# Performance work log

Hardware: AMD Instinct MI355X
Metric: run time of the kernel (lower is better)

The kernel has to match this reference:

```python
import jax, jax.numpy as jnp
import numpy as np

B, S_Q, S_KV = 4, 2048, 2048
D_MODEL, HEADS, D_QK, D_V = 1024, 16, 64, 64


def setup_inputs() -> dict:
    key = jax.random.key(0)
    ks = jax.random.split(key, 12)
    s = lambda fan_in: 1.0 / np.sqrt(fan_in)
    return {
        "x": jax.random.normal(ks[0], (B, S_Q, D_MODEL), jnp.float32),
        "encoder_output": jax.random.normal(ks[1], (B, S_KV, D_MODEL), jnp.float32),
        # per-head Linear weights stacked over heads: [H, D_MODEL, d_head]
        "Wq": jax.random.uniform(ks[2], (HEADS, D_MODEL, D_QK), jnp.float32, -s(D_MODEL), s(D_MODEL)),
        "bq": jax.random.uniform(ks[3], (HEADS, D_QK), jnp.float32, -s(D_MODEL), s(D_MODEL)),
        "Wk": jax.random.uniform(ks[4], (HEADS, D_MODEL, D_QK), jnp.float32, -s(D_MODEL), s(D_MODEL)),
        "bk": jax.random.uniform(ks[5], (HEADS, D_QK), jnp.float32, -s(D_MODEL), s(D_MODEL)),
        "Wv": jax.random.uniform(ks[6], (HEADS, D_MODEL, D_V), jnp.float32, -s(D_MODEL), s(D_MODEL)),
        "bv": jax.random.uniform(ks[7], (HEADS, D_V), jnp.float32, -s(D_MODEL), s(D_MODEL)),
        # output Linear: [H*D_V, D_MODEL]
        "Wo": jax.random.uniform(ks[8], (HEADS * D_V, D_MODEL), jnp.float32, -s(HEADS * D_V), s(HEADS * D_V)),
        "bo": jax.random.uniform(ks[9], (D_MODEL,), jnp.float32, -s(HEADS * D_V), s(HEADS * D_V)),
    }


def reference(x, encoder_output, Wq, bq, Wk, bk, Wv, bv, Wo, bo):
    # Batched equivalent of the per-head Python loop: project all heads at once.
    q = jnp.einsum("bqd,hde->bhqe", x, Wq) + bq[None, :, None, :]              # [B,H,Sq,dk]
    k = jnp.einsum("bsd,hde->bhse", encoder_output, Wk) + bk[None, :, None, :]  # [B,H,Skv,dk]
    v = jnp.einsum("bsd,hde->bhse", encoder_output, Wv) + bv[None, :, None, :]  # [B,H,Skv,dv]
    scale = 1.0 / jnp.sqrt(jnp.asarray(D_QK, x.dtype))
    scores = jnp.einsum("bhqe,bhse->bhqs", q, k) * scale                        # [B,H,Sq,Skv]
    attn = jax.nn.softmax(scores, axis=-1)
    heads = jnp.einsum("bhqs,bhse->bhqe", attn, v)                              # [B,H,Sq,dv]
    # concat heads on last dim (head order matches the torch list concat)
    multihead = heads.transpose(0, 2, 1, 3).reshape(x.shape[0], x.shape[1], HEADS * D_V)
    return multihead @ Wo + bo
```

## Files before the change

kernel.cpp:

```cpp
#include <hip/hip_runtime.h>
#include <hip/hip_bf16.h>
#include <stdint.h>

typedef unsigned short u16;
typedef __bf16 bf16x8 __attribute__((ext_vector_type(8)));
typedef float f32x4 __attribute__((ext_vector_type(4)));
typedef float f32x16 __attribute__((ext_vector_type(16)));
typedef unsigned short us8 __attribute__((ext_vector_type(8)));

__device__ __forceinline__ u16 f2bf(float f) {
  union { float f; uint32_t u; } v; v.f = f;
  uint32_t u = v.u;
  return (u16)((u + 0x7FFFu + ((u >> 16) & 1u)) >> 16);
}

__device__ __forceinline__ uint32_t cvtpk(float a, float b) {
  uint32_t r;
  asm("v_cvt_pk_bf16_f32 %0, %1, %2" : "=v"(r) : "v"(a), "v"(b));
  return r;
}

__device__ __forceinline__ void gload_lds16(const void* g, void* l) {
  __builtin_amdgcn_global_load_lds(
      (const __attribute__((address_space(1))) void*)(uintptr_t)g,
      (__attribute__((address_space(3))) void*)(uint32_t)(uintptr_t)l,
      16, 0, 0);
}

__device__ __forceinline__ float vsum16(f32x16 v) {
  float a = (v[0] + v[1]) + (v[2] + v[3]);
  float b = (v[4] + v[5]) + (v[6] + v[7]);
  float c = (v[8] + v[9]) + (v[10] + v[11]);
  float d = (v[12] + v[13]) + (v[14] + v[15]);
  return (a + b) + (c + d);
}

#define CROW(r, g) (((r) & 3) + 8 * ((r) >> 2) + 4 * (g))


__global__ __launch_bounds__(256) void f32_to_bf16_k(const float* __restrict__ in,
                                                     u16* __restrict__ out) {
  size_t i = (size_t)blockIdx.x * 256 + threadIdx.x;
  const float4* p = (const float4*)in + i * 2;
  float4 a = p[0], b = p[1];
  us8 o;
  o[0] = f2bf(a.x); o[1] = f2bf(a.y); o[2] = f2bf(a.z); o[3] = f2bf(a.w);
  o[4] = f2bf(b.x); o[5] = f2bf(b.y); o[6] = f2bf(b.z); o[7] = f2bf(b.w);
  *(us8*)(out + i * 8) = o;
}

__global__ __launch_bounds__(256) void cvt_wqkv_k(const float* __restrict__ Wq,
                                                  const float* __restrict__ Wk,
                                                  const float* __restrict__ Wv,
                                                  u16* __restrict__ oq, u16* __restrict__ ok,
                                                  u16* __restrict__ ov) {
  __shared__ float t[64][65];
  int z = blockIdx.z;
  const float* W = (z == 0) ? Wq : (z == 1) ? Wk : Wv;
  u16* o = (z == 0) ? oq : (z == 1) ? ok : ov;
  const int h = blockIdx.y, d0 = blockIdx.x * 64;
  const int tid = threadIdx.x;
  const float* Wb = W + ((size_t)h << 16) + (size_t)d0 * 64;
#pragma unroll
  for (int i = 0; i < 4; ++i) {
    int idx = tid + i * 256;
    int dl = idx >> 4, e4 = (idx & 15) << 2;
    float4 v = *(const float4*)(Wb + dl * 64 + e4);
    t[dl][e4 + 0] = v.x; t[dl][e4 + 1] = v.y; t[dl][e4 + 2] = v.z; t[dl][e4 + 3] = v.w;
  }
  __syncthreads();
#pragma unroll
  for (int i = 0; i < 2; ++i) {
    int idx = tid + i * 256;
    int e = idx >> 3, dc = (idx & 7) * 8;
    us8 w;
#pragma unroll
    for (int j = 0; j < 8; ++j) w[j] = f2bf(t[dc + j][e]);
    *(us8*)(o + ((size_t)(h * 64 + e)) * 1024 + d0 + dc) = w;
  }
}

__global__ __launch_bounds__(256) void cvt_wo_k(const float* __restrict__ Wo,
                                                u16* __restrict__ o) {
  __shared__ float t[64][65];
  const int k0 = blockIdx.x * 64, n0 = blockIdx.y * 64;
  const int tid = threadIdx.x;
  const float* Wb = Wo + (size_t)k0 * 1024 + n0;
#pragma unroll
  for (int i = 0; i < 4; ++i) {
    int idx = tid + i * 256;
    int kl = idx >> 4, n4 = (idx & 15) << 2;
    float4 v = *(const float4*)(Wb + (size_t)kl * 1024 + n4);
    t[kl][n4 + 0] = v.x; t[kl][n4 + 1] = v.y; t[kl][n4 + 2] = v.z; t[kl][n4 + 3] = v.w;
  }
  __syncthreads();
#pragma unroll
  for (int i = 0; i < 2; ++i) {
    int idx = tid + i * 256;
    int n = idx >> 3, kc = (idx & 7) * 8;
    us8 w;
#pragma unroll
    for (int j = 0; j < 8; ++j) w[j] = f2bf(t[kc + j][n]);
    *(us8*)(o + ((size_t)(n0 + n)) * 1024 + k0 + kc) = w;
  }
}

template <int MODE>
__global__ __launch_bounds__(256) void gemm_bt_k(const u16* __restrict__ A,
                                                 const u16* __restrict__ B,
                                                 const float* __restrict__ bias,
                                                 void* __restrict__ C, int M, int N, int K,
                                                 float scale) {
  __shared__ __attribute__((aligned(16))) u16 As[128 * 32];
  __shared__ __attribute__((aligned(16))) u16 Bs[128 * 32];
  const int tid = threadIdx.x;
  const int wave = tid >> 6, lane = tid & 63;
  const int lo = lane & 15, hi = lane >> 4;
  const int n0 = blockIdx.x * 128, m0 = blockIdx.y * 128;
  const int wr = wave >> 1, wc = wave & 1;

  f32x4 acc[4][4] = {};

  const int o0 = wave * 1024 + lane * 16;
  const int r0 = o0 >> 6, cb0 = o0 & 63;
  const int o1 = o0 + 4096;
  const int r1 = o1 >> 6, cb1 = o1 & 63;

  const char* Ac = (const char*)A;
  const char* Bc = (const char*)B;

  for (int kk = 0; kk < K; kk += 32) {
    __syncthreads();
    gload_lds16(Ac + ((size_t)(m0 + r0) * K + kk) * 2 + cb0, (char*)As + o0);
    gload_lds16(Ac + ((size_t)(m0 + r1) * K + kk) * 2 + cb1, (char*)As + o1);
    gload_lds16(Bc + ((size_t)(n0 + r0) * K + kk) * 2 + cb0, (char*)Bs + o0);
    gload_lds16(Bc + ((size_t)(n0 + r1) * K + kk) * 2 + cb1, (char*)Bs + o1);
    __syncthreads();
    bf16x8 af[4], bfr[4];
#pragma unroll
    for (int i = 0; i < 4; ++i) {
      af[i]  = *(const bf16x8*)(As + (wr * 64 + i * 16 + lo) * 32 + hi * 8);
      bfr[i] = *(const bf16x8*)(Bs + (wc * 64 + i * 16 + lo) * 32 + hi * 8);
    }
#pragma unroll
    for (int am = 0; am < 4; ++am)
#pragma unroll
      for (int bn = 0; bn < 4; ++bn)
        acc[am][bn] = __builtin_amdgcn_mfma_f32_16x16x32_bf16(af[am], bfr[bn], acc[am][bn], 0, 0, 0);
  }

  if constexpr (MODE == 0) {
    u16* Co = (u16*)C;
#pragma unroll
    for (int bn = 0; bn < 4; ++bn) {
      int col = n0 + wc * 64 + bn * 16 + lo;
      float bb = bias[col];
      int hh = col >> 6, e = col & 63;
#pragma unroll
      for (int am = 0; am < 4; ++am) {
#pragma unroll
        for (int r = 0; r < 4; ++r) {
          int row = m0 + wr * 64 + am * 16 + hi * 4 + r;
          int b = row >> 11, s = row & 2047;
          Co[(((size_t)(b * 16 + hh) * 2048 + s) << 6) + e] = f2bf((acc[am][bn][r] + bb) * scale);
        }
      }
    }
  } else {
    float* Cf = (float*)C;
#pragma unroll
    for (int bn = 0; bn < 4; ++bn) {
      int col = n0 + wc * 64 + bn * 16 + lo;
      float bb = bias[col];
#pragma unroll
      for (int am = 0; am < 4; ++am) {
#pragma unroll
        for (int r = 0; r < 4; ++r) {
          int row = m0 + wr * 64 + am * 16 + hi * 4 + r;
          Cf[(size_t)row * N + col] = acc[am][bn][r] + bb;
        }
      }
    }
  }
}

__global__ __launch_bounds__(256) void gemm_kv_k(const u16* __restrict__ A,
                                                 const u16* __restrict__ Bkv,
                                                 const float* __restrict__ bk_,
                                                 const float* __restrict__ bv_,
                                                 u16* __restrict__ Kg, u16* __restrict__ Vg,
                                                 int M, int K) {
  __shared__ __attribute__((aligned(16))) u16 As[128 * 32];
  __shared__ __attribute__((aligned(16))) u16 Bs[128 * 32];
  const int tid = threadIdx.x;
  const int wave = tid >> 6, lane = tid & 63;
  const int lo = lane & 15, hi = lane >> 4;
  const int n0 = blockIdx.x * 128, m0 = blockIdx.y * 128;
  const int wr = wave >> 1, wc = wave & 1;

  f32x4 acc[4][4] = {};

  const int o0 = wave * 1024 + lane * 16;
  const int r0 = o0 >> 6, cb0 = o0 & 63;
  const int o1 = o0 + 4096;
  const int r1 = o1 >> 6, cb1 = o1 & 63;

  const char* Ac = (const char*)A;
  const char* Bc = (const char*)Bkv;

  for (int kk = 0; kk < K; kk += 32) {
    __syncthreads();
    gload_lds16(Ac + ((size_t)(m0 + r0) * K + kk) * 2 + cb0, (char*)As + o0);
    gload_lds16(Ac + ((size_t)(m0 + r1) * K + kk) * 2 + cb1, (char*)As + o1);
    gload_lds16(Bc + ((size_t)(n0 + r0) * K + kk) * 2 + cb0, (char*)Bs + o0);
    gload_lds16(Bc + ((size_t)(n0 + r1) * K + kk) * 2 + cb1, (char*)Bs + o1);
    __syncthreads();
    bf16x8 af[4], bfr[4];
#pragma unroll
    for (int i = 0; i < 4; ++i) {
      af[i]  = *(const bf16x8*)(As + (wr * 64 + i * 16 + lo) * 32 + hi * 8);
      bfr[i] = *(const bf16x8*)(Bs + (wc * 64 + i * 16 + lo) * 32 + hi * 8);
    }
#pragma unroll
    for (int am = 0; am < 4; ++am)
#pragma unroll
      for (int bn = 0; bn < 4; ++bn)
        acc[am][bn] = __builtin_amdgcn_mfma_f32_16x16x32_bf16(af[am], bfr[bn], acc[am][bn], 0, 0, 0);
  }

  const bool isV = (n0 + wc * 64) >= 1024;
  u16* dst = isV ? Vg : Kg;
#pragma unroll
  for (int bn = 0; bn < 4; ++bn) {
    int col = (n0 + wc * 64 + bn * 16 + lo) & 1023;
    float bb = isV ? bv_[col] : bk_[col];
    int hh = col >> 6, e = col & 63;
#pragma unroll
    for (int am = 0; am < 4; ++am) {
#pragma unroll
      for (int r = 0; r < 4; ++r) {
        int row = m0 + wr * 64 + am * 16 + hi * 4 + r;
        int b = row >> 11, s = row & 2047;
        if (!isV) s = (s & ~12) | ((s & 4) << 1) | ((s & 8) >> 1);
        dst[(((size_t)(b * 16 + hh) * 2048 + s) << 6) + e] = f2bf(acc[am][bn][r] + bb);
      }
    }
  }
}

__global__ __launch_bounds__(256) void transpose_v_k(const u16* __restrict__ V,
                                                     u16* __restrict__ Vt) {
  __shared__ __attribute__((aligned(16))) u16 t[64][72];
  const int bh = blockIdx.y;
  const int s0 = blockIdx.x * 64;
  const int tid = threadIdx.x;
  const u16* Vb = V + ((size_t)bh * 2048 + s0) * 64;
#pragma unroll
  for (int i = 0; i < 2; ++i) {
    int c = tid + i * 256;
    int s = c >> 3, e0 = (c & 7) * 8;
    us8 d = *(const us8*)(Vb + s * 64 + e0);
#pragma unroll
    for (int j = 0; j < 8; ++j) t[e0 + j][s] = d[j];
  }
  __syncthreads();
  u16* Vo = Vt + ((size_t)bh * 64) * 2048 + s0;
#pragma unroll
  for (int i = 0; i < 2; ++i) {
    int c = tid + i * 256;
    int e = c >> 3, sb = (c & 7) * 8;
    *(us8*)(Vo + (size_t)e * 2048 + sb) = *(const us8*)(&t[e][sb]);
  }
}

__global__ __launch_bounds__(256, 4) void attn_k(const u16* __restrict__ Qg,
                                                 const u16* __restrict__ Kg,
                                                 const u16* __restrict__ Vtg,
                                                 u16* __restrict__ Hd) {
  const int W = blockIdx.x;
  const int bid = (W >> 7) * 128 + (W & 7) * 16 + ((W >> 3) & 15);
  const int bh = bid >> 4;
  const int q0 = (bid & 15) * 128;
  const int tid = threadIdx.x;
  const int w = tid >> 6, lane = tid & 63;
  const int q31 = lane & 31, g = lane >> 5;

  __shared__ __attribute__((aligned(16))) char LB[2][16384];

  bf16x8 qf0, qf1, qf2, qf3;
  {
    const char* Qrow = (const char*)(Qg + ((size_t)bh * 2048 + q0 + w * 32 + q31) * 64) + g * 16;
    qf0 = *(const bf16x8*)(Qrow);
    qf1 = *(const bf16x8*)(Qrow + 32);
    qf2 = *(const bf16x8*)(Qrow + 64);
    qf3 = *(const bf16x8*)(Qrow + 96);
  }

  f32x16 acc0 = {}, acc1 = {};
  float lrun = 0.f;

  const int lrow = lane >> 3;
  const int scol = ((lane & 7) ^ lrow) << 4;
  const char* kp = (const char*)Kg + (size_t)bh * 262144 + (size_t)(w * 16 + lrow) * 128 + scol;
  const char* vp = (const char*)Vtg + (size_t)bh * 262144 + (size_t)(w * 16 + lrow) * 4096 + scol;

  auto STAGE = [&](int c) {
    char* kb = &LB[c][0] + w * 2048;
    char* vb = kb + 8192;
    gload_lds16(kp, kb);
    gload_lds16(kp + 1024, kb + 1024);
    gload_lds16(vp, vb);
    gload_lds16(vp + 32768, vb + 1024);
    kp += 8192;
    vp += 128;
  };

  STAGE(0);

  const int swz = (q31 & 7) << 4;
  const int krow = q31 * 128;
  const int ko0 = (g * 16) ^ swz;
  const int ko1 = (32 + g * 16) ^ swz;
  const int ko2 = (64 + g * 16) ^ swz;
  const int ko3 = (96 + g * 16) ^ swz;

  int cur = 0;
  for (int t = 0; t < 32; ++t) {
    asm volatile("s_waitcnt vmcnt(0)" ::: "memory");
    __builtin_amdgcn_s_barrier();
    asm volatile("" ::: "memory");
    if (t < 31) STAGE(cur ^ 1);

    const char* Kc = &LB[cur][0];
    const char* Vc = Kc + 8192;

    f32x16 p0 = {}, p1 = {};
    __builtin_amdgcn_s_setprio(1);
    {
      bf16x8 kf;
      kf = *(const bf16x8*)(Kc + krow + ko0);
      p0 = __builtin_amdgcn_mfma_f32_32x32x16_bf16(kf, qf0, p0, 0, 0, 0);
      kf = *(const bf16x8*)(Kc + 4096 + krow + ko0);
      p1 = __builtin_amdgcn_mfma_f32_32x32x16_bf16(kf, qf0, p1, 0, 0, 0);
      kf = *(const bf16x8*)(Kc + krow + ko1);
      p0 = __builtin_amdgcn_mfma_f32_32x32x16_bf16(kf, qf1, p0, 0, 0, 0);
      kf = *(const bf16x8*)(Kc + 4096 + krow + ko1);
      p1 = __builtin_amdgcn_mfma_f32_32x32x16_bf16(kf, qf1, p1, 0, 0, 0);
      kf = *(const bf16x8*)(Kc + krow + ko2);
      p0 = __builtin_amdgcn_mfma_f32_32x32x16_bf16(kf, qf2, p0, 0, 0, 0);
      kf = *(const bf16x8*)(Kc + 4096 + krow + ko2);
      p1 = __builtin_amdgcn_mfma_f32_32x32x16_bf16(kf, qf2, p1, 0, 0, 0);
      kf = *(const bf16x8*)(Kc + krow + ko3);
      p0 = __builtin_amdgcn_mfma_f32_32x32x16_bf16(kf, qf3, p0, 0, 0, 0);
      kf = *(const bf16x8*)(Kc + 4096 + krow + ko3);
      p1 = __builtin_amdgcn_mfma_f32_32x32x16_bf16(kf, qf3, p1, 0, 0, 0);
    }
    __builtin_amdgcn_s_setprio(0);

#pragma unroll
    for (int i = 0; i < 16; ++i) p0[i] = __builtin_amdgcn_exp2f(p0[i]);
#pragma unroll
    for (int i = 0; i < 16; ++i) p1[i] = __builtin_amdgcn_exp2f(p1[i]);

    float rs = vsum16(p0) + vsum16(p1);
    {
      float ra = rs, rb = rs;
      asm("v_permlane32_swap_b32 %0, %1" : "+v"(ra), "+v"(rb));
      rs += g ? ra : rb;
    }
    lrun += rs;

    union PU { uint32_t u[4]; bf16x8 v; } a0, a1, a2, a3;
    a0.u[0] = cvtpk(p0[0], p0[1]);   a0.u[1] = cvtpk(p0[2], p0[3]);
    a0.u[2] = cvtpk(p0[4], p0[5]);   a0.u[3] = cvtpk(p0[6], p0[7]);
    a1.u[0] = cvtpk(p0[8], p0[9]);   a1.u[1] = cvtpk(p0[10], p0[11]);
    a1.u[2] = cvtpk(p0[12], p0[13]); a1.u[3] = cvtpk(p0[14], p0[15]);
    a2.u[0] = cvtpk(p1[0], p1[1]);   a2.u[1] = cvtpk(p1[2], p1[3]);
    a2.u[2] = cvtpk(p1[4], p1[5]);   a2.u[3] = cvtpk(p1[6], p1[7]);
    a3.u[0] = cvtpk(p1[8], p1[9]);   a3.u[1] = cvtpk(p1[10], p1[11]);
    a3.u[2] = cvtpk(p1[12], p1[13]); a3.u[3] = cvtpk(p1[14], p1[15]);

    __builtin_amdgcn_s_setprio(1);
    {
      bf16x8 vf;
      vf = *(const bf16x8*)(Vc + krow + ko0);
      acc0 = __builtin_amdgcn_mfma_f32_32x32x16_bf16(a0.v, vf, acc0, 0, 0, 0);
      vf = *(const bf16x8*)(Vc + 4096 + krow + ko0);
      acc1 = __builtin_amdgcn_mfma_f32_32x32x16_bf16(a0.v, vf, acc1, 0, 0, 0);
      vf = *(const bf16x8*)(Vc + krow + ko1);
      acc0 = __builtin_amdgcn_mfma_f32_32x32x16_bf16(a1.v, vf, acc0, 0, 0, 0);
      vf = *(const bf16x8*)(Vc + 4096 + krow + ko1);
      acc1 = __builtin_amdgcn_mfma_f32_32x32x16_bf16(a1.v, vf, acc1, 0, 0, 0);
      vf = *(const bf16x8*)(Vc + krow + ko2);
      acc0 = __builtin_amdgcn_mfma_f32_32x32x16_bf16(a2.v, vf, acc0, 0, 0, 0);
      vf = *(const bf16x8*)(Vc + 4096 + krow + ko2);
      acc1 = __builtin_amdgcn_mfma_f32_32x32x16_bf16(a2.v, vf, acc1, 0, 0, 0);
      vf = *(const bf16x8*)(Vc + krow + ko3);
      acc0 = __builtin_amdgcn_mfma_f32_32x32x16_bf16(a3.v, vf, acc0, 0, 0, 0);
      vf = *(const bf16x8*)(Vc + 4096 + krow + ko3);
      acc1 = __builtin_amdgcn_mfma_f32_32x32x16_bf16(a3.v, vf, acc1, 0, 0, 0);
    }
    __builtin_amdgcn_s_setprio(0);

    cur ^= 1;
  }

  float linv = 1.f / lrun;
  const int b = bh >> 4, h = bh & 15;
  u16* Ho = Hd + ((size_t)b * 2048 + q0 + w * 32) * 1024 + h * 64;
#pragma unroll
  for (int r = 0; r < 16; ++r) {
    float iv = __shfl(linv, CROW(r, g));
    int q = CROW(r, g);
    u16* row = Ho + (size_t)q * 1024;
    row[q31]      = f2bf(acc0[r] * iv);
    row[32 + q31] = f2bf(acc1[r] * iv);
  }
}


extern "C" void kernel_launch(void* const* d_in, const int* in_sizes, int n_in,
                              void* d_out, int out_size, void* d_ws, size_t ws_size,
                              hipStream_t stream) {
  const float* x   = (const float*)d_in[0];
  const float* enc = (const float*)d_in[1];
  const float* Wq  = (const float*)d_in[2];
  const float* bq  = (const float*)d_in[3];
  const float* Wk  = (const float*)d_in[4];
  const float* bk  = (const float*)d_in[5];
  const float* Wv  = (const float*)d_in[6];
  const float* bv  = (const float*)d_in[7];
  const float* Wo  = (const float*)d_in[8];
  const float* bo  = (const float*)d_in[9];
  float* out = (float*)d_out;
  char* ws = (char*)d_ws;

  const size_t SZ = 16u * 1024u * 1024u;
  u16* xb  = (u16*)(ws + 0 * SZ);
  u16* eb  = (u16*)(ws + 1 * SZ);
  u16* Qg  = (u16*)(ws + 2 * SZ);
  u16* Kg  = (u16*)(ws + 3 * SZ);
  u16* Vg  = (u16*)(ws + 4 * SZ);
  u16* wqb = (u16*)(ws + 5 * SZ + 0u * (2u << 20));
  u16* wkb = (u16*)(ws + 5 * SZ + 1u * (2u << 20));
  u16* wvb = (u16*)(ws + 5 * SZ + 2u * (2u << 20));
  u16* wob = (u16*)(ws + 5 * SZ + 3u * (2u << 20));
  u16* hd  = xb;
  u16* vtb = eb;

  const float cs = 0.18033688011112042f;

  f32_to_bf16_k<<<4096, 256, 0, stream>>>(x, xb);
  f32_to_bf16_k<<<4096, 256, 0, stream>>>(enc, eb);
  cvt_wqkv_k<<<dim3(16, 16, 3), 256, 0, stream>>>(Wq, Wk, Wv, wqb, wkb, wvb);
  cvt_wo_k<<<dim3(16, 16), 256, 0, stream>>>(Wo, wob);

  gemm_bt_k<0><<<dim3(8, 64), 256, 0, stream>>>(xb, wqb, bq, Qg, 8192, 1024, 1024, cs);
  gemm_kv_k<<<dim3(16, 64), 256, 0, stream>>>(eb, wkb, bk, bv, Kg, Vg, 8192, 1024);

  transpose_v_k<<<dim3(32, 64), 256, 0, stream>>>(Vg, vtb);
  attn_k<<<1024, 256, 0, stream>>>(Qg, Kg, vtb, hd);

  gemm_bt_k<1><<<dim3(8, 64), 256, 0, stream>>>(hd, wob, bo, out, 8192, 1024, 1024, 1.0f);
}
```

Baseline: 232.4 us.

## Double-buffer GEMM LDS loads, fuse conversions, write V transposed from GEMM epilogue

Merges the four f32-to-bf16 conversion kernels into one launch and removes the separate V transpose kernel by having the K/V GEMM epilogue write V directly in transposed layout. The GEMM main loop now double-buffers LDS with asynchronous global-to-LDS loads, waits on vmcnt, prefetches two stages ahead and raises wave priority around the MFMAs. This is meant to overlap memory latency with compute and cut launch and extra-pass traffic. In exchange it doubles LDS use per block and the transposed V stores are narrow 8-byte strided writes.

```diff
diff --git a/kernel.cpp b/kernel.cpp
--- a/kernel.cpp
+++ b/kernel.cpp
@@ -37,71 +37,78 @@
 
 #define CROW(r, g) (((r) & 3) + 8 * ((r) >> 2) + 4 * (g))
 
-
-__global__ __launch_bounds__(256) void f32_to_bf16_k(const float* __restrict__ in,
-                                                     u16* __restrict__ out) {
-  size_t i = (size_t)blockIdx.x * 256 + threadIdx.x;
-  const float4* p = (const float4*)in + i * 2;
-  float4 a = p[0], b = p[1];
-  us8 o;
-  o[0] = f2bf(a.x); o[1] = f2bf(a.y); o[2] = f2bf(a.z); o[3] = f2bf(a.w);
-  o[4] = f2bf(b.x); o[5] = f2bf(b.y); o[6] = f2bf(b.z); o[7] = f2bf(b.w);
-  *(us8*)(out + i * 8) = o;
-}
-
-__global__ __launch_bounds__(256) void cvt_wqkv_k(const float* __restrict__ Wq,
-                                                  const float* __restrict__ Wk,
-                                                  const float* __restrict__ Wv,
-                                                  u16* __restrict__ oq, u16* __restrict__ ok,
-                                                  u16* __restrict__ ov) {
+__global__ __launch_bounds__(256) void cvt_all_k(
+    const float* __restrict__ x, const float* __restrict__ enc,
+    const float* __restrict__ Wq, const float* __restrict__ Wk,
+    const float* __restrict__ Wv, const float* __restrict__ Wo,
+    u16* __restrict__ xb, u16* __restrict__ eb,
+    u16* __restrict__ wqb, u16* __restrict__ wkb,
+    u16* __restrict__ wvb, u16* __restrict__ wob) {
   __shared__ float t[64][65];
-  int z = blockIdx.z;
-  const float* W = (z == 0) ? Wq : (z == 1) ? Wk : Wv;
-  u16* o = (z == 0) ? oq : (z == 1) ? ok : ov;
-  const int h = blockIdx.y, d0 = blockIdx.x * 64;
+  const int blk = blockIdx.x;
   const int tid = threadIdx.x;
-  const float* Wb = W + ((size_t)h << 16) + (size_t)d0 * 64;
-#pragma unroll
-  for (int i = 0; i < 4; ++i) {
-    int idx = tid + i * 256;
-    int dl = idx >> 4, e4 = (idx & 15) << 2;
-    float4 v = *(const float4*)(Wb + dl * 64 + e4);
-    t[dl][e4 + 0] = v.x; t[dl][e4 + 1] = v.y; t[dl][e4 + 2] = v.z; t[dl][e4 + 3] = v.w;
-  }
-  __syncthreads();
-#pragma unroll
-  for (int i = 0; i < 2; ++i) {
-    int idx = tid + i * 256;
-    int e = idx >> 3, dc = (idx & 7) * 8;
-    us8 w;
-#pragma unroll
-    for (int j = 0; j < 8; ++j) w[j] = f2bf(t[dc + j][e]);
-    *(us8*)(o + ((size_t)(h * 64 + e)) * 1024 + d0 + dc) = w;
-  }
-}
-
-__global__ __launch_bounds__(256) void cvt_wo_k(const float* __restrict__ Wo,
-                                                u16* __restrict__ o) {
-  __shared__ float t[64][65];
-  const int k0 = blockIdx.x * 64, n0 = blockIdx.y * 64;
-  const int tid = threadIdx.x;
-  const float* Wb = Wo + (size_t)k0 * 1024 + n0;
-#pragma unroll
-  for (int i = 0; i < 4; ++i) {
-    int idx = tid + i * 256;
-    int kl = idx >> 4, n4 = (idx & 15) << 2;
-    float4 v = *(const float4*)(Wb + (size_t)kl * 1024 + n4);
-    t[kl][n4 + 0] = v.x; t[kl][n4 + 1] = v.y; t[kl][n4 + 2] = v.z; t[kl][n4 + 3] = v.w;
-  }
-  __syncthreads();
-#pragma unroll
-  for (int i = 0; i < 2; ++i) {
-    int idx = tid + i * 256;
-    int n = idx >> 3, kc = (idx & 7) * 8;
-    us8 w;
-#pragma unroll
-    for (int j = 0; j < 8; ++j) w[j] = f2bf(t[kc + j][n]);
-    *(us8*)(o + ((size_t)(n0 + n)) * 1024 + k0 + kc) = w;
+
+  if (blk < 8192) {
+    const float* in = (blk < 4096) ? x : enc;
+    u16* out = (blk < 4096) ? xb : eb;
+    size_t i = (size_t)(blk & 4095) * 256 + tid;
+    const float4* p = (const float4*)in + i * 2;
+    float4 a = p[0], b = p[1];
+    us8 o;
+    o[0] = f2bf(a.x); o[1] = f2bf(a.y); o[2] = f2bf(a.z); o[3] = f2bf(a.w);
+    o[4] = f2bf(b.x); o[5] = f2bf(b.y); o[6] = f2bf(b.z); o[7] = f2bf(b.w);
+    *(us8*)(out + i * 8) = o;
+    return;
+  }
+
+  if (blk < 8960) {
+    int r = blk - 8192;
+    int z = r >> 8;
+    const float* W = (z == 0) ? Wq : (z == 1) ? Wk : Wv;
+    u16* o = (z == 0) ? wqb : (z == 1) ? wkb : wvb;
+    const int h = (r & 255) >> 4, d0 = (r & 15) * 64;
+    const float* Wb = W + ((size_t)h << 16) + (size_t)d0 * 64;
+#pragma unroll
+    for (int i = 0; i < 4; ++i) {
+      int idx = tid + i * 256;
+      int dl = idx >> 4, e4 = (idx & 15) << 2;
+      float4 v = *(const float4*)(Wb + dl * 64 + e4);
+      t[dl][e4 + 0] = v.x; t[dl][e4 + 1] = v.y; t[dl][e4 + 2] = v.z; t[dl][e4 + 3] = v.w;
+    }
+    __syncthreads();
+#pragma unroll
+    for (int i = 0; i < 2; ++i) {
+      int idx = tid + i * 256;
+      int e = idx >> 3, dc = (idx & 7) * 8;
+      us8 w;
+#pragma unroll
+      for (int j = 0; j < 8; ++j) w[j] = f2bf(t[dc + j][e]);
+      *(us8*)(o + ((size_t)(h * 64 + e)) * 1024 + d0 + dc) = w;
+    }
+    return;
+  }
+
+  {
+    int r = blk - 8960;
+    const int k0 = (r & 15) * 64, n0 = (r >> 4) * 64;
+    const float* Wb = Wo + (size_t)k0 * 1024 + n0;
+#pragma unroll
+    for (int i = 0; i < 4; ++i) {
+      int idx = tid + i * 256;
+      int kl = idx >> 4, n4 = (idx & 15) << 2;
+      float4 v = *(const float4*)(Wb + (size_t)kl * 1024 + n4);
+      t[kl][n4 + 0] = v.x; t[kl][n4 + 1] = v.y; t[kl][n4 + 2] = v.z; t[kl][n4 + 3] = v.w;
+    }
+    __syncthreads();
+#pragma unroll
+    for (int i = 0; i < 2; ++i) {
+      int idx = tid + i * 256;
+      int n = idx >> 3, kc = (idx & 7) * 8;
+      us8 w;
+#pragma unroll
+      for (int j = 0; j < 8; ++j) w[j] = f2bf(t[kc + j][n]);
+      *(us8*)(wob + ((size_t)(n0 + n)) * 1024 + k0 + kc) = w;
+    }
   }
 }
 
@@ -109,10 +116,11 @@
 __global__ __launch_bounds__(256) void gemm_bt_k(const u16* __restrict__ A,
                                                  const u16* __restrict__ B,
                                                  const float* __restrict__ bias,
-                                                 void* __restrict__ C, int M, int N, int K,
-                                                 float scale) {
-  __shared__ __attribute__((aligned(16))) u16 As[128 * 32];
-  __shared__ __attribute__((aligned(16))) u16 Bs[128 * 32];
+                                                 const float* __restrict__ bias2,
+                                                 void* __restrict__ C, void* __restrict__ C2,
+                                                 int M, int N, int K, float scale) {
+  __shared__ __attribute__((aligned(16))) u16 As[2][128 * 32];
+  __shared__ __attribute__((aligned(16))) u16 Bs[2][128 * 32];
   const int tid = threadIdx.x;
   const int wave = tid >> 6, lane = tid & 63;
   const int lo = lane & 15, hi = lane >> 4;
@@ -128,25 +136,49 @@
 
   const char* Ac = (const char*)A;
   const char* Bc = (const char*)B;
-
-  for (int kk = 0; kk < K; kk += 32) {
-    __syncthreads();
-    gload_lds16(Ac + ((size_t)(m0 + r0) * K + kk) * 2 + cb0, (char*)As + o0);
-    gload_lds16(Ac + ((size_t)(m0 + r1) * K + kk) * 2 + cb1, (char*)As + o1);
-    gload_lds16(Bc + ((size_t)(n0 + r0) * K + kk) * 2 + cb0, (char*)Bs + o0);
-    gload_lds16(Bc + ((size_t)(n0 + r1) * K + kk) * 2 + cb1, (char*)Bs + o1);
-    __syncthreads();
+  const size_t ksz = (size_t)K * 2;
+
+  auto STAGE = [&](int t) {
+    const size_t kb = (size_t)t * 64;
+    char* Ad = (char*)As[t & 1];
+    char* Bd = (char*)Bs[t & 1];
+    gload_lds16(Ac + (size_t)(m0 + r0) * ksz + kb + cb0, Ad + o0);
+    gload_lds16(Ac + (size_t)(m0 + r1) * ksz + kb + cb1, Ad + o1);
+    gload_lds16(Bc + (size_t)(n0 + r0) * ksz + kb + cb0, Bd + o0);
+    gload_lds16(Bc + (size_t)(n0 + r1) * ksz + kb + cb1, Bd + o1);
+  };
+
+  const int NK = K >> 5;
+  STAGE(0);
+  STAGE(1);
+
+  for (int kk = 0; kk < NK; ++kk) {
+    if (kk < NK - 1) {
+      asm volatile("s_waitcnt vmcnt(4)" ::: "memory");
+    } else {
+      asm volatile("s_waitcnt vmcnt(0)" ::: "memory");
+    }
+    __builtin_amdgcn_s_barrier();
+    __builtin_amdgcn_sched_barrier(0);
+    const u16* Asb = As[kk & 1];
+    const u16* Bsb = Bs[kk & 1];
     bf16x8 af[4], bfr[4];
 #pragma unroll
     for (int i = 0; i < 4; ++i) {
-      af[i]  = *(const bf16x8*)(As + (wr * 64 + i * 16 + lo) * 32 + hi * 8);
-      bfr[i] = *(const bf16x8*)(Bs + (wc * 64 + i * 16 + lo) * 32 + hi * 8);
-    }
+      af[i]  = *(const bf16x8*)(Asb + (wr * 64 + i * 16 + lo) * 32 + hi * 8);
+      bfr[i] = *(const bf16x8*)(Bsb + (wc * 64 + i * 16 + lo) * 32 + hi * 8);
+    }
+    asm volatile("s_waitcnt lgkmcnt(0)" ::: "memory");
+    __builtin_amdgcn_sched_barrier(0);
+    __builtin_amdgcn_s_barrier();
+    if (kk + 2 < NK) STAGE(kk + 2);
+    __builtin_amdgcn_s_setprio(1);
 #pragma unroll
     for (int am = 0; am < 4; ++am)
 #pragma unroll
       for (int bn = 0; bn < 4; ++bn)
         acc[am][bn] = __builtin_amdgcn_mfma_f32_16x16x32_bf16(af[am], bfr[bn], acc[am][bn], 0, 0, 0);
+    __builtin_amdgcn_s_setprio(0);
   }
 
   if constexpr (MODE == 0) {
@@ -166,7 +198,7 @@
         }
       }
     }
-  } else {
+  } else if constexpr (MODE == 1) {
     float* Cf = (float*)C;
 #pragma unroll
     for (int bn = 0; bn < 4; ++bn) {
@@ -181,95 +213,44 @@
         }
       }
     }
-  }
-}
-
-__global__ __launch_bounds__(256) void gemm_kv_k(const u16* __restrict__ A,
-                                                 const u16* __restrict__ Bkv,
-                                                 const float* __restrict__ bk_,
-                                                 const float* __restrict__ bv_,
-                                                 u16* __restrict__ Kg, u16* __restrict__ Vg,
-                                                 int M, int K) {
-  __shared__ __attribute__((aligned(16))) u16 As[128 * 32];
-  __shared__ __attribute__((aligned(16))) u16 Bs[128 * 32];
-  const int tid = threadIdx.x;
-  const int wave = tid >> 6, lane = tid & 63;
-  const int lo = lane & 15, hi = lane >> 4;
-  const int n0 = blockIdx.x * 128, m0 = blockIdx.y * 128;
-  const int wr = wave >> 1, wc = wave & 1;
-
-  f32x4 acc[4][4] = {};
-
-  const int o0 = wave * 1024 + lane * 16;
-  const int r0 = o0 >> 6, cb0 = o0 & 63;
-  const int o1 = o0 + 4096;
-  const int r1 = o1 >> 6, cb1 = o1 & 63;
-
-  const char* Ac = (const char*)A;
-  const char* Bc = (const char*)Bkv;
-
-  for (int kk = 0; kk < K; kk += 32) {
-    __syncthreads();
-    gload_lds16(Ac + ((size_t)(m0 + r0) * K + kk) * 2 + cb0, (char*)As + o0);
-    gload_lds16(Ac + ((size_t)(m0 + r1) * K + kk) * 2 + cb1, (char*)As + o1);
-    gload_lds16(Bc + ((size_t)(n0 + r0) * K + kk) * 2 + cb0, (char*)Bs + o0);
-    gload_lds16(Bc + ((size_t)(n0 + r1) * K + kk) * 2 + cb1, (char*)Bs + o1);
-    __syncthreads();
-    bf16x8 af[4], bfr[4];
-#pragma unroll
-    for (int i = 0; i < 4; ++i) {
-      af[i]  = *(const bf16x8*)(As + (wr * 64 + i * 16 + lo) * 32 + hi * 8);
-      bfr[i] = *(const bf16x8*)(Bs + (wc * 64 + i * 16 + lo) * 32 + hi * 8);
-    }
-#pragma unroll
-    for (int am = 0; am < 4; ++am)
-#pragma unroll
-      for (int bn = 0; bn < 4; ++bn)
-        acc[am][bn] = __builtin_amdgcn_mfma_f32_16x16x32_bf16(af[am], bfr[bn], acc[am][bn], 0, 0, 0);
-  }
-
-  const bool isV = (n0 + wc * 64) >= 1024;
-  u16* dst = isV ? Vg : Kg;
-#pragma unroll
-  for (int bn = 0; bn < 4; ++bn) {
-    int col = (n0 + wc * 64 + bn * 16 + lo) & 1023;
-    float bb = isV ? bv_[col] : bk_[col];
-    int hh = col >> 6, e = col & 63;
-#pragma unroll
-    for (int am = 0; am < 4; ++am) {
-#pragma unroll
-      for (int r = 0; r < 4; ++r) {
-        int row = m0 + wr * 64 + am * 16 + hi * 4 + r;
-        int b = row >> 11, s = row & 2047;
-        if (!isV) s = (s & ~12) | ((s & 4) << 1) | ((s & 8) >> 1);
-        dst[(((size_t)(b * 16 + hh) * 2048 + s) << 6) + e] = f2bf(acc[am][bn][r] + bb);
+  } else {
+    const bool isV = (n0 + wc * 64) >= 1024;
+    if (!isV) {
+      u16* Co = (u16*)C;
+#pragma unroll
+      for (int bn = 0; bn < 4; ++bn) {
+        int col = n0 + wc * 64 + bn * 16 + lo;
+        float bb = bias[col];
+        int hh = col >> 6, e = col & 63;
+#pragma unroll
+        for (int am = 0; am < 4; ++am) {
+#pragma unroll
+          for (int r = 0; r < 4; ++r) {
+            int row = m0 + wr * 64 + am * 16 + hi * 4 + r;
+            int b = row >> 11, s = row & 2047;
+            s = (s & ~12) | ((s & 4) << 1) | ((s & 8) >> 1);
+            Co[(((size_t)(b * 16 + hh) * 2048 + s) << 6) + e] = f2bf(acc[am][bn][r] + bb);
+          }
+        }
       }
-    }
-  }
-}
-
-__global__ __launch_bounds__(256) void transpose_v_k(const u16* __restrict__ V,
-                                                     u16* __restrict__ Vt) {
-  __shared__ __attribute__((aligned(16))) u16 t[64][72];
-  const int bh = blockIdx.y;
-  const int s0 = blockIdx.x * 64;
-  const int tid = threadIdx.x;
-  const u16* Vb = V + ((size_t)bh * 2048 + s0) * 64;
-#pragma unroll
-  for (int i = 0; i < 2; ++i) {
-    int c = tid + i * 256;
-    int s = c >> 3, e0 = (c & 7) * 8;
-    us8 d = *(const us8*)(Vb + s * 64 + e0);
-#pragma unroll
-    for (int j = 0; j < 8; ++j) t[e0 + j][s] = d[j];
-  }
-  __syncthreads();
-  u16* Vo = Vt + ((size_t)bh * 64) * 2048 + s0;
-#pragma unroll
-  for (int i = 0; i < 2; ++i) {
-    int c = tid + i * 256;
-    int e = c >> 3, sb = (c & 7) * 8;
-    *(us8*)(Vo + (size_t)e * 2048 + sb) = *(const us8*)(&t[e][sb]);
+    } else {
+      u16* Vt = (u16*)C2;
+#pragma unroll
+      for (int bn = 0; bn < 4; ++bn) {
+        int c = (n0 + wc * 64 + bn * 16 + lo) - 1024;
+        float bb = bias2[c];
+        int hh = c >> 6, e = c & 63;
+#pragma unroll
+        for (int am = 0; am < 4; ++am) {
+          int row = m0 + wr * 64 + am * 16 + hi * 4;
+          int b = row >> 11, s = row & 2047;
+          uint2 wv;
+          wv.x = cvtpk(acc[am][bn][0] + bb, acc[am][bn][1] + bb);
+          wv.y = cvtpk(acc[am][bn][2] + bb, acc[am][bn][3] + bb);
+          *(uint2*)(Vt + (((size_t)(b * 16 + hh) * 64 + e) * 2048 + s)) = wv;
+        }
+      }
+    }
   }
 }
 
@@ -440,26 +421,24 @@
   u16* eb  = (u16*)(ws + 1 * SZ);
   u16* Qg  = (u16*)(ws + 2 * SZ);
   u16* Kg  = (u16*)(ws + 3 * SZ);
-  u16* Vg  = (u16*)(ws + 4 * SZ);
+  u16* vtb = (u16*)(ws + 4 * SZ);
   u16* wqb = (u16*)(ws + 5 * SZ + 0u * (2u << 20));
   u16* wkb = (u16*)(ws + 5 * SZ + 1u * (2u << 20));
   u16* wvb = (u16*)(ws + 5 * SZ + 2u * (2u << 20));
   u16* wob = (u16*)(ws + 5 * SZ + 3u * (2u << 20));
   u16* hd  = xb;
-  u16* vtb = eb;
 
   const float cs = 0.18033688011112042f;
 
-  f32_to_bf16_k<<<4096, 256, 0, stream>>>(x, xb);
-  f32_to_bf16_k<<<4096, 256, 0, stream>>>(enc, eb);
-  cvt_wqkv_k<<<dim3(16, 16, 3), 256, 0, stream>>>(Wq, Wk, Wv, wqb, wkb, wvb);
-  cvt_wo_k<<<dim3(16, 16), 256, 0, stream>>>(Wo, wob);
-
-  gemm_bt_k<0><<<dim3(8, 64), 256, 0, stream>>>(xb, wqb, bq, Qg, 8192, 1024, 1024, cs);
-  gemm_kv_k<<<dim3(16, 64), 256, 0, stream>>>(eb, wkb, bk, bv, Kg, Vg, 8192, 1024);
-
-  transpose_v_k<<<dim3(32, 64), 256, 0, stream>>>(Vg, vtb);
+  cvt_all_k<<<9216, 256, 0, stream>>>(x, enc, Wq, Wk, Wv, Wo, xb, eb, wqb, wkb, wvb, wob);
+
+  gemm_bt_k<0><<<dim3(8, 64), 256, 0, stream>>>(xb, wqb, bq, nullptr, Qg, nullptr,
+                                                8192, 1024, 1024, cs);
+  gemm_bt_k<2><<<dim3(16, 64), 256, 0, stream>>>(eb, wkb, bk, bv, Kg, vtb,
+                                                 8192, 2048, 1024, 1.0f);
+
   attn_k<<<1024, 256, 0, stream>>>(Qg, Kg, vtb, hd);
 
-  gemm_bt_k<1><<<dim3(8, 64), 256, 0, stream>>>(hd, wob, bo, out, 8192, 1024, 1024, 1.0f);
-}
+  gemm_bt_k<1><<<dim3(8, 64), 256, 0, stream>>>(hd, wob, bo, nullptr, out, nullptr,
+                                                8192, 1024, 1024, 1.0f);
+}
```

Result: faster. 201.7 us (-13.2%).
